# Optimization experiments

Hardware: AMD Instinct MI355X
Metric: run time of the kernel (lower is better)

## Reference

```python
import jax, jax.numpy as jnp
import numpy as np

N = 100000   # total nodes
E = 1000000  # edges
D = 64       # input_dim
H = 128      # embed_dim


def setup_inputs() -> dict:
    key = jax.random.key(0)
    k1, k2, k3, k4 = jax.random.split(key, 4)
    nodes = jnp.arange(N, dtype=jnp.int32)
    features = jax.random.normal(k1, (N, D), dtype=jnp.float32)
    edge_index = jax.random.randint(k2, (2, E), 0, N, dtype=jnp.int32)
    # nn.Linear(2*D, H): weight [H, 2D], bias [H]
    W = jax.random.normal(k3, (H, 2 * D), dtype=jnp.float32) / np.sqrt(2 * D)
    b = jax.random.normal(k4, (H,), dtype=jnp.float32) * 0.01
    return {"nodes": nodes, "features": features, "edge_index": edge_index,
            "W": W, "b": b}


def reference(nodes, features, edge_index, W, b):
    src, dst = edge_index[0], edge_index[1]
    # gcn=False: neighbors are undirected (both src->dst and dst->src).
    # Mean aggregator over all neighbors (full-neighborhood mean).
    ones = jnp.ones((E,), dtype=features.dtype)
    neigh_sum = (jax.ops.segment_sum(features[dst], src, num_segments=N)
                 + jax.ops.segment_sum(features[src], dst, num_segments=N))
    deg = (jax.ops.segment_sum(ones, src, num_segments=N)
           + jax.ops.segment_sum(ones, dst, num_segments=N))
    neigh_mean = neigh_sum / jnp.maximum(deg, 1.0)[:, None]  # [N, D]
    self_feats = features[nodes]            # [B, D]
    neigh_feats = neigh_mean[nodes]         # [B, D]
    combined = jnp.concatenate([self_feats, neigh_feats], axis=1)  # [B, 2D]
    out = jax.nn.relu(combined @ W.T + b)   # [B, H]
    return out
```

## Files before the change

### kernel.cpp

```cpp
#include <hip/hip_runtime.h>
#include <hip/hip_bf16.h>


#define D_IN 64
#define H_OUT 128
#define CAP 64
#define CAP_L 61
#define NPB 32
#define BSHIFT 8
#define BUK_N 256
#define NBUK_MAX 512
#define PASSA_BLOCKS 256
#define PASSA_THREADS 512

typedef unsigned long long ull;
typedef unsigned short ushortt;
typedef unsigned char uchar;
typedef __attribute__((ext_vector_type(8))) short bf16x8;
typedef __attribute__((ext_vector_type(4))) float f32x4;
typedef __attribute__((ext_vector_type(2))) float f32x2;

__device__ __forceinline__ ushortt f2bf(float f) {
    __hip_bfloat16 h = __float2bfloat16(f);
    return *reinterpret_cast<ushortt*>(&h);
}
__device__ __forceinline__ float bf2f(ushortt u) {
    unsigned int x = ((unsigned int)u) << 16;
    return __uint_as_float(x);
}

__global__ __launch_bounds__(PASSA_THREADS) void prep_kernel(
    const int* __restrict__ ei,
    unsigned* __restrict__ gbuf,
    int* __restrict__ blkcnt,
    const float4* __restrict__ feat4,
    const float4* __restrict__ w4,
    ushortt* __restrict__ fb,
    uint2* __restrict__ fq,
    ushortt* __restrict__ Wb,
    int E, int nbuk, int scap, int chunk, int nfeat8, int nw8)
{
    const int t = threadIdx.x;

    if (blockIdx.x >= PASSA_BLOCKS) {
        int i = (blockIdx.x - PASSA_BLOCKS) * PASSA_THREADS + t;
        if (i < nfeat8) {
            float4 a = feat4[2 * i], b = feat4[2 * i + 1];
            bf16x8 o;
            o[0] = (short)f2bf(a.x); o[1] = (short)f2bf(a.y);
            o[2] = (short)f2bf(a.z); o[3] = (short)f2bf(a.w);
            o[4] = (short)f2bf(b.x); o[5] = (short)f2bf(b.y);
            o[6] = (short)f2bf(b.z); o[7] = (short)f2bf(b.w);
            *(bf16x8*)&fb[(size_t)i * 8] = o;
            unsigned lo = (unsigned)__builtin_amdgcn_cvt_pk_fp8_f32(a.x, a.y, 0, false);
            lo = (unsigned)__builtin_amdgcn_cvt_pk_fp8_f32(a.z, a.w, (int)lo, true);
            unsigned hi = (unsigned)__builtin_amdgcn_cvt_pk_fp8_f32(b.x, b.y, 0, false);
            hi = (unsigned)__builtin_amdgcn_cvt_pk_fp8_f32(b.z, b.w, (int)hi, true);
            uint2 q; q.x = lo; q.y = hi;
            fq[i] = q;
        } else {
            int j = i - nfeat8;
            if (j < nw8) {
                float4 a = w4[2 * j], b = w4[2 * j + 1];
                bf16x8 o;
                o[0] = (short)f2bf(a.x); o[1] = (short)f2bf(a.y);
                o[2] = (short)f2bf(a.z); o[3] = (short)f2bf(a.w);
                o[4] = (short)f2bf(b.x); o[5] = (short)f2bf(b.y);
                o[6] = (short)f2bf(b.z); o[7] = (short)f2bf(b.w);
                *(bf16x8*)&Wb[(size_t)j * 8] = o;
            }
        }
        return;
    }

    __shared__ int lcnt[NBUK_MAX];
    for (int i = t; i < nbuk; i += PASSA_THREADS) lcnt[i] = 0;
    __syncthreads();

    const int E2 = 2 * E;
    int lo = blockIdx.x * chunk;
    int hi = lo + chunk; if (hi > E2) hi = E2;

    for (int i = lo + t; i < hi; i += PASSA_THREADS) {
        int u = ei[i];
        int v = (i < E) ? ei[E + i] : ei[i - E];
        int b = u >> BSHIFT;
        unsigned pk = ((unsigned)v << BSHIFT) | (unsigned)(u & (BUK_N - 1));
        int p = atomicAdd(&lcnt[b], 1);
        if (p < scap) gbuf[((size_t)blockIdx.x * nbuk + b) * scap + p] = pk;
    }
    __syncthreads();
    for (int b = t; b < nbuk; b += PASSA_THREADS)
        blkcnt[blockIdx.x * nbuk + b] = lcnt[b];
}

__global__ __launch_bounds__(1024) void adj_agg_kernel(
    const unsigned* __restrict__ gbuf,
    const int* __restrict__ blkcnt,
    const int* __restrict__ ei,
    const uchar* __restrict__ fq,
    ushortt* __restrict__ meanb,
    int N, int E, int nbuk, int scap)
{
    __shared__ unsigned adj_l[BUK_N * CAP_L];
    __shared__ int cnt_l[BUK_N];
    __shared__ int scnt_l[PASSA_BLOCKS];
    __shared__ int satf;

    const int b = blockIdx.x;
    const int t = threadIdx.x;

    if (t == 0) satf = 0;
    if (t < BUK_N) cnt_l[t] = 0;
    if (t < PASSA_BLOCKS) {
        int c = blkcnt[t * nbuk + b];
        scnt_l[t] = c;
        if (c > scap) satf = 1;
    }
    __syncthreads();

    const int wv   = t >> 6;
    const int lane = t & 63;

    if (satf) {
        const int E2 = 2 * E;
        for (int i = t; i < E2; i += 1024) {
            int u = ei[i];
            if ((u >> BSHIFT) != b) continue;
            int v = (i < E) ? ei[E + i] : ei[i - E];
            int ul = u & (BUK_N - 1);
            int p  = atomicAdd(&cnt_l[ul], 1);
            if (p < CAP_L) adj_l[ul * CAP_L + p] = (unsigned)v;
        }
    } else {
        for (int seg = wv; seg < PASSA_BLOCKS; seg += 16) {
            int c = scnt_l[seg]; if (c > scap) c = scap;
            const unsigned* base = gbuf + ((size_t)seg * nbuk + b) * scap;
            for (int i = lane; i < c; i += 64) {
                unsigned e = base[i];
                int ul = e & (BUK_N - 1);
                int v  = (int)(e >> BSHIFT);
                int p  = atomicAdd(&cnt_l[ul], 1);
                if (p < CAP_L) adj_l[ul * CAP_L + p] = (unsigned)v;
            }
        }
    }
    __syncthreads();

    const int oct = lane >> 3;
    const int ol  = lane & 7;
    const uchar* fqb = fq + ol * 8;

    const int nbase = wv * 16;
    const int gbase = (b << BSHIFT) + nbase;

#define GATH(U0, U1, U2, U3, AROW, CC)                                       \
    {                                                                        \
        if ((CC) > 0) {                                                      \
            int jj = oct;      int a = jj < (CC);                            \
            unsigned id = (AROW)[a ? jj : 0];                                \
            U0 = *(const uint2*)(fqb + (size_t)(id * 64u));                  \
            if (!a) { U0.x = 0u; U0.y = 0u; }                                \
        }                                                                    \
        if ((CC) > 8) {                                                      \
            int jj = 8 + oct;  int a = jj < (CC);                            \
            unsigned id = (AROW)[a ? jj : 0];                                \
            U1 = *(const uint2*)(fqb + (size_t)(id * 64u));                  \
            if (!a) { U1.x = 0u; U1.y = 0u; }                                \
        }                                                                    \
        if ((CC) > 16) {                                                     \
            int jj = 16 + oct; int a = jj < (CC);                            \
            unsigned id = (AROW)[a ? jj : 0];                                \
            U2 = *(const uint2*)(fqb + (size_t)(id * 64u));                  \
            if (!a) { U2.x = 0u; U2.y = 0u; }                                \
        }                                                                    \
        if ((CC) > 24) {                                                     \
            int jj = 24 + oct; int a = jj < (CC);                            \
            unsigned id = (AROW)[a ? jj : 0];                                \
            U3 = *(const uint2*)(fqb + (size_t)(id * 64u));                  \
            if (!a) { U3.x = 0u; U3.y = 0u; }                                \
        }                                                                    \
    }

#define DEC(u)                                                       \
    s0 += __builtin_amdgcn_cvt_pk_f32_fp8((int)(u).x, false);        \
    s1 += __builtin_amdgcn_cvt_pk_f32_fp8((int)(u).x, true);         \
    s2 += __builtin_amdgcn_cvt_pk_f32_fp8((int)(u).y, false);        \
    s3 += __builtin_amdgcn_cvt_pk_f32_fp8((int)(u).y, true);

#define FINISH(UA, UB, UC, UD, CC, CTRUE, AROW, G)                           \
    {                                                                        \
        f32x2 s0 = {0.f, 0.f}, s1 = {0.f, 0.f};                              \
        f32x2 s2 = {0.f, 0.f}, s3 = {0.f, 0.f};                              \
        DEC(UA); DEC(UB); DEC(UC); DEC(UD);                                  \
        if (__builtin_expect((CC) > 32, 0)) {                                \
            for (int j = 32; j < (CC); j += 8) {                             \
                int jj = j + oct; int a = jj < (CC);                         \
                unsigned id = (AROW)[a ? jj : 0];                            \
                uint2 u = *(const uint2*)(fqb + (size_t)(id * 64u));         \
                if (!a) { u.x = 0u; u.y = 0u; }                              \
                DEC(u);                                                      \
            }                                                                \
        }                                                                    \
        f32x2 a0, a1;                                                        \
        {                                                                    \
            f32x2 t0, t1, t2, t3;                                            \
            t0.x = __shfl_xor(s0.x, 8);  t0.y = __shfl_xor(s0.y, 8);         \
            t1.x = __shfl_xor(s1.x, 8);  t1.y = __shfl_xor(s1.y, 8);         \
            t2.x = __shfl_xor(s2.x, 8);  t2.y = __shfl_xor(s2.y, 8);         \
            t3.x = __shfl_xor(s3.x, 8);  t3.y = __shfl_xor(s3.y, 8);         \
            bool hi = (oct & 1);                                             \
            a0 = hi ? (s2 + t2) : (s0 + t0);                                 \
            a1 = hi ? (s3 + t3) : (s1 + t1);                                 \
        }                                                                    \
        f32x2 b0;                                                            \
        {                                                                    \
            f32x2 t0, t1;                                                    \
            t0.x = __shfl_xor(a0.x, 16); t0.y = __shfl_xor(a0.y, 16);        \
            t1.x = __shfl_xor(a1.x, 16); t1.y = __shfl_xor(a1.y, 16);        \
            bool hi = (oct & 2);                                             \
            b0 = hi ? (a1 + t1) : (a0 + t0);                                 \
        }                                                                    \
        float cf;                                                            \
        {                                                                    \
            f32x2 tt;                                                        \
            tt.x = __shfl_xor(b0.x, 32); tt.y = __shfl_xor(b0.y, 32);        \
            f32x2 ss = b0 + tt;                                              \
            cf = (oct & 4) ? ss.y : ss.x;                                    \
        }                                                                    \
        float r = 1.0f / fmaxf((float)(CTRUE), 1.0f);                        \
        int d = 8 * ol + 4 * (oct & 1) + (oct & 2) + ((oct >> 2) & 1);       \
        meanb[(size_t)(G) * D_IN + d] = f2bf(cf * r);                        \
    }

    for (int np = 0; np < 8; ++np) {
        const int n0 = nbase + 2 * np;
        const int g0 = gbase + 2 * np;
        const int g1 = g0 + 1;

        const int c0  = (g0 < N) ? cnt_l[n0] : 0;
        const int c1  = (g1 < N) ? cnt_l[n0 + 1] : 0;
        const int cc0 = c0 < CAP_L ? c0 : CAP_L;
        const int cc1 = c1 < CAP_L ? c1 : CAP_L;
        const unsigned* ar0 = &adj_l[n0 * CAP_L];
        const unsigned* ar1 = &adj_l[(n0 + 1) * CAP_L];

        uint2 u00 = {0u,0u}, u01 = {0u,0u}, u02 = {0u,0u}, u03 = {0u,0u};
        uint2 u10 = {0u,0u}, u11 = {0u,0u}, u12 = {0u,0u}, u13 = {0u,0u};
        GATH(u00, u01, u02, u03, ar0, cc0);
        GATH(u10, u11, u12, u13, ar1, cc1);

        if (g0 < N) FINISH(u00, u01, u02, u03, cc0, c0, ar0, g0);
        if (g1 < N) FINISH(u10, u11, u12, u13, cc1, c1, ar1, g1);
    }
#undef GATH
#undef DEC
#undef FINISH
}

__global__ __launch_bounds__(256) void build_adj_kernel(
    const int* __restrict__ ei,
    int* __restrict__ cnt,
    int* __restrict__ adj,
    int E)
{
    const int part   = blockIdx.x & 7;
    const int bloc   = blockIdx.x >> 3;
    const int nbp    = gridDim.x >> 3;
    const int stride = nbp * 256;
    const int E2     = 2 * E;

    for (int i = bloc * 256 + (int)threadIdx.x; i < E2; i += stride) {
        int u = ei[i];
        if (((u >> 4) & 7) != part) continue;
        int v = (i < E) ? ei[E + i] : ei[i - E];
        int p = atomicAdd(&cnt[u], 1);
        if (p < CAP_L) adj[u * CAP + p] = v;
    }
}

__global__ __launch_bounds__(256) void aggregate_f32_kernel(
    const float* __restrict__ feat,
    const int* __restrict__ adj,
    const int* __restrict__ cnt,
    ushortt* __restrict__ meanb,
    int N)
{
    int wid  = (blockIdx.x * blockDim.x + threadIdx.x) >> 6;
    int lane = threadIdx.x & 63;
    if (wid >= N) return;

    int c  = cnt[wid];
    int cc = c < CAP_L ? c : CAP_L;
    int ids = adj[wid * CAP + lane];

    float sum = 0.0f;
    int j = 0;
    for (; j + 8 <= cc; j += 8) {
        int i0 = __shfl(ids, j + 0);
        int i1 = __shfl(ids, j + 1);
        int i2 = __shfl(ids, j + 2);
        int i3 = __shfl(ids, j + 3);
        int i4 = __shfl(ids, j + 4);
        int i5 = __shfl(ids, j + 5);
        int i6 = __shfl(ids, j + 6);
        int i7 = __shfl(ids, j + 7);
        float f0 = feat[i0 * D_IN + lane];
        float f1 = feat[i1 * D_IN + lane];
        float f2 = feat[i2 * D_IN + lane];
        float f3 = feat[i3 * D_IN + lane];
        float f4 = feat[i4 * D_IN + lane];
        float f5 = feat[i5 * D_IN + lane];
        float f6 = feat[i6 * D_IN + lane];
        float f7 = feat[i7 * D_IN + lane];
        sum += ((f0 + f1) + (f2 + f3)) + ((f4 + f5) + (f6 + f7));
    }
    for (; j < cc; ++j)
        sum += feat[__shfl(ids, j) * D_IN + lane];

    float m = sum / fmaxf((float)c, 1.0f);
    meanb[(size_t)wid * D_IN + lane] = f2bf(m);
}

__global__ __launch_bounds__(256) void gemm_mfma_kernel(
    const int* __restrict__ nodes,
    const ushortt* __restrict__ fb,
    const ushortt* __restrict__ meanb,
    const ushortt* __restrict__ Wb,
    const float* __restrict__ bias,
    float* __restrict__ out,
    int N)
{
    __shared__ ushortt w_lds[128 * 136];
    __shared__ int gnode[64];

    const int t  = threadIdx.x;
    const int n0 = blockIdx.x * 64;

    if (t < 64) {
        int idx = n0 + t;
        gnode[t] = nodes[idx < N ? idx : N - 1];
    }
    for (int i = t; i < 128 * 16; i += 256) {
        int row = i >> 4, seg = i & 15;
        *(bf16x8*)&w_lds[row * 136 + seg * 8] =
            *(const bf16x8*)&Wb[row * 128 + seg * 8];
    }
    __syncthreads();

    const int w    = t >> 6;
    const int lane = t & 63;
    const int l15  = lane & 15;
    const int quad = lane >> 4;

    const int g = gnode[w * 16 + l15];
    const bf16x8 a0 = *(const bf16x8*)&fb[(size_t)g * D_IN +  0 + quad * 8];
    const bf16x8 a1 = *(const bf16x8*)&fb[(size_t)g * D_IN + 32 + quad * 8];
    const bf16x8 a2 = *(const bf16x8*)&meanb[(size_t)g * D_IN +  0 + quad * 8];
    const bf16x8 a3 = *(const bf16x8*)&meanb[(size_t)g * D_IN + 32 + quad * 8];

    const int  out_row = n0 + w * 16 + l15;
    const bool valid   = out_row < N;

#pragma unroll
    for (int tile = 0; tile < 8; ++tile) {
        const int h0 = tile * 16;
        const ushortt* wrow = &w_lds[(h0 + l15) * 136];
        bf16x8 b0 = *(const bf16x8*)&wrow[ 0 + quad * 8];
        bf16x8 b1 = *(const bf16x8*)&wrow[32 + quad * 8];
        bf16x8 b2 = *(const bf16x8*)&wrow[64 + quad * 8];
        bf16x8 b3 = *(const bf16x8*)&wrow[96 + quad * 8];

        f32x4 acc = {0.f, 0.f, 0.f, 0.f};
        acc = __builtin_amdgcn_mfma_f32_16x16x32_bf16(b0, a0, acc, 0, 0, 0);
        acc = __builtin_amdgcn_mfma_f32_16x16x32_bf16(b1, a1, acc, 0, 0, 0);
        acc = __builtin_amdgcn_mfma_f32_16x16x32_bf16(b2, a2, acc, 0, 0, 0);
        acc = __builtin_amdgcn_mfma_f32_16x16x32_bf16(b3, a3, acc, 0, 0, 0);

        if (valid) {
            float4 bv = *(const float4*)&bias[h0 + quad * 4];
            float4 o;
            o.x = fmaxf(acc[0] + bv.x, 0.0f);
            o.y = fmaxf(acc[1] + bv.y, 0.0f);
            o.z = fmaxf(acc[2] + bv.z, 0.0f);
            o.w = fmaxf(acc[3] + bv.w, 0.0f);
            *(float4*)&out[(size_t)out_row * H_OUT + h0 + quad * 4] = o;
        }
    }
}

__global__ __launch_bounds__(256) void gemm_kernel(
    const int* __restrict__ nodes,
    const float* __restrict__ feat,
    const ushortt* __restrict__ meanb,
    const float* __restrict__ W,
    const float* __restrict__ bias,
    float* __restrict__ out,
    int N)
{
    __shared__ float w_lds[64 * 132];
    __shared__ float comb_self[NPB * 68];
    __shared__ float comb_mean[NPB * 68];
    __shared__ int   gnode[NPB];

    const int t  = threadIdx.x;
    const int n0 = blockIdx.x * NPB;

    if (t < NPB) {
        int idx = n0 + t;
        if (idx >= N) idx = N - 1;
        gnode[t] = nodes[idx];
    }
    __syncthreads();

    for (int i = t; i < NPB * 64; i += 256) {
        int n = i >> 6, d = i & 63;
        int g = gnode[n];
        comb_self[n * 68 + d] = feat[g * D_IN + d];
        comb_mean[n * 68 + d] = bf2f(meanb[(size_t)g * D_IN + d]);
    }
    for (int i = t; i < H_OUT * 64; i += 256) {
        int h = i >> 6, kk = i & 63;
        w_lds[kk * 132 + h] = W[h * (2 * D_IN) + kk];
    }
    __syncthreads();

    const int tx = t & 31;
    const int ty = t >> 5;
    const int h0 = tx * 4;
    const int nl = ty * 4;

    float acc[4][4];
#pragma unroll
    for (int j = 0; j < 4; j++)
#pragma unroll
        for (int i = 0; i < 4; i++) acc[j][i] = 0.0f;

    for (int kk = 0; kk < 64; kk += 4) {
        float4 wvv[4], cv[4];
#pragma unroll
        for (int i = 0; i < 4; i++)
            wvv[i] = *(const float4*)&w_lds[(kk + i) * 132 + h0];
#pragma unroll
        for (int j = 0; j < 4; j++)
            cv[j] = *(const float4*)&comb_self[(nl + j) * 68 + kk];
#pragma unroll
        for (int j = 0; j < 4; j++) {
            const float* c = (const float*)&cv[j];
#pragma unroll
            for (int i = 0; i < 4; i++) {
                const float* wp = (const float*)&wvv[i];
                acc[j][0] += wp[0] * c[i];
                acc[j][1] += wp[1] * c[i];
                acc[j][2] += wp[2] * c[i];
                acc[j][3] += wp[3] * c[i];
            }
        }
    }
    __syncthreads();

    for (int i = t; i < H_OUT * 64; i += 256) {
        int h = i >> 6, kk = i & 63;
        w_lds[kk * 132 + h] = W[h * (2 * D_IN) + 64 + kk];
    }
    __syncthreads();

    for (int kk = 0; kk < 64; kk += 4) {
        float4 wvv[4], cv[4];
#pragma unroll
        for (int i = 0; i < 4; i++)
            wvv[i] = *(const float4*)&w_lds[(kk + i) * 132 + h0];
#pragma unroll
        for (int j = 0; j < 4; j++)
            cv[j] = *(const float4*)&comb_mean[(nl + j) * 68 + kk];
#pragma unroll
        for (int j = 0; j < 4; j++) {
            const float* c = (const float*)&cv[j];
#pragma unroll
            for (int i = 0; i < 4; i++) {
                const float* wp = (const float*)&wvv[i];
                acc[j][0] += wp[0] * c[i];
                acc[j][1] += wp[1] * c[i];
                acc[j][2] += wp[2] * c[i];
                acc[j][3] += wp[3] * c[i];
            }
        }
    }

    float4 bv = *(const float4*)&bias[h0];
#pragma unroll
    for (int j = 0; j < 4; j++) {
        int n = n0 + nl + j;
        if (n >= N) continue;
        float4 o;
        o.x = fmaxf(acc[j][0] + bv.x, 0.0f);
        o.y = fmaxf(acc[j][1] + bv.y, 0.0f);
        o.z = fmaxf(acc[j][2] + bv.z, 0.0f);
        o.w = fmaxf(acc[j][3] + bv.w, 0.0f);
        *(float4*)&out[(size_t)n * H_OUT + h0] = o;
    }
}

extern "C" void kernel_launch(void* const* d_in, const int* in_sizes, int n_in,
                              void* d_out, int out_size, void* d_ws, size_t ws_size,
                              hipStream_t stream) {
    const int*   nodes = (const int*)d_in[0];
    const float* feat  = (const float*)d_in[1];
    const int*   ei    = (const int*)d_in[2];
    const float* W     = (const float*)d_in[3];
    const float* bias  = (const float*)d_in[4];
    float*       out   = (float*)d_out;

    const int N  = in_sizes[0];
    const int E  = in_sizes[2] / 2;
    const int E2 = 2 * E;

    const int nbuk  = (N + BUK_N - 1) >> BSHIFT;
    const int chunk = (E2 + PASSA_BLOCKS - 1) / PASSA_BLOCKS;
    double ex = (double)chunk * (double)BUK_N / (double)N;
    int scap = ((int)(ex + 9.0 * __builtin_sqrt(ex)) + 31) & ~15;
    if (scap < 64) scap = 64;

    char* base = (char*)d_ws;
    size_t off = 0;
    auto aln = [](size_t x) { return (x + 63) & ~(size_t)63; };
    int*     cnt    = (int*)(base + off);     off = aln(off + (size_t)N * 4);
    int*     adj    = (int*)(base + off);     off = aln(off + (size_t)N * CAP * 4);
    ushortt* meanb  = (ushortt*)(base + off); off = aln(off + (size_t)N * D_IN * 2);
    int*     blkcnt = (int*)(base + off);     off = aln(off + (size_t)PASSA_BLOCKS * NBUK_MAX * 4);
    ushortt* Wb     = (ushortt*)(base + off); off = aln(off + (size_t)H_OUT * 2 * D_IN * 2);
    ushortt* fb     = (ushortt*)(base + off); off = aln(off + (size_t)N * D_IN * 2);
    uchar*   fq     = (uchar*)(base + off);   off = aln(off + (size_t)N * D_IN);
    unsigned* gbuf  = (unsigned*)(base + off);
    const size_t total = off + (size_t)PASSA_BLOCKS * nbuk * scap * 4;

    const bool full = (N <= 131072) && (nbuk <= NBUK_MAX) && (ws_size >= total)
                   && ((N * D_IN) % 8 == 0);

    if (full) {
        const int nfeat8 = N * D_IN / 8;
        const int nw8    = H_OUT * 2 * D_IN / 8;
        const int conv_blocks = (nfeat8 + nw8 + PASSA_THREADS - 1) / PASSA_THREADS;
        prep_kernel<<<PASSA_BLOCKS + conv_blocks, PASSA_THREADS, 0, stream>>>(
            ei, gbuf, blkcnt, (const float4*)feat, (const float4*)W,
            fb, (uint2*)fq, Wb, E, nbuk, scap, chunk, nfeat8, nw8);
        adj_agg_kernel<<<nbuk, 1024, 0, stream>>>(gbuf, blkcnt, ei, fq,
                                                  meanb, N, E, nbuk, scap);
        gemm_mfma_kernel<<<(N + 63) / 64, 256, 0, stream>>>(
            nodes, fb, meanb, Wb, bias, out, N);
    } else {
        const int ablocks = (int)(((size_t)N * 64 + 255) / 256);
        hipMemsetAsync(cnt, 0, (size_t)N * sizeof(int), stream);
        build_adj_kernel<<<2048, 256, 0, stream>>>(ei, cnt, adj, E);
        aggregate_f32_kernel<<<ablocks, 256, 0, stream>>>(feat, adj, cnt,
                                                          meanb, N);
        gemm_kernel<<<(N + NPB - 1) / NPB, 256, 0, stream>>>(
            nodes, feat, meanb, W, bias, out, N);
    }
}
```

Measured before the change: 169.9 us.

## Fuse output GEMM into aggregation kernel with identity-nodes fast path and backup

```diff
diff --git a/kernel.cpp b/kernel.cpp
--- a/kernel.cpp
+++ b/kernel.cpp
@@ -38,9 +38,11 @@
     ushortt* __restrict__ fb,
     uint2* __restrict__ fq,
     ushortt* __restrict__ Wb,
+    int* __restrict__ flag,
     int E, int nbuk, int scap, int chunk, int nfeat8, int nw8)
 {
     const int t = threadIdx.x;
+    if (blockIdx.x == 0 && t == 0) *flag = 0;
 
     if (blockIdx.x >= PASSA_BLOCKS) {
         int i = (blockIdx.x - PASSA_BLOCKS) * PASSA_THREADS + t;
@@ -94,12 +96,18 @@
         blkcnt[blockIdx.x * nbuk + b] = lcnt[b];
 }
 
-__global__ __launch_bounds__(1024) void adj_agg_kernel(
+__global__ __launch_bounds__(1024, 8) void adj_agg_kernel(
     const unsigned* __restrict__ gbuf,
     const int* __restrict__ blkcnt,
     const int* __restrict__ ei,
     const uchar* __restrict__ fq,
     ushortt* __restrict__ meanb,
+    const int* __restrict__ nodes,
+    const ushortt* __restrict__ fb,
+    const ushortt* __restrict__ Wb,
+    const float* __restrict__ bias,
+    float* __restrict__ out,
+    int* __restrict__ flag,
     int N, int E, int nbuk, int scap)
 {
     __shared__ unsigned adj_l[BUK_N * CAP_L];
@@ -256,6 +264,128 @@
 #undef GATH
 #undef DEC
 #undef FINISH
+
+    __threadfence();
+    __syncthreads();
+    {
+        const int grp   = t >> 8;
+        const int t256  = t & 255;
+        const int w2    = t256 >> 6;
+        const int lane2 = t256 & 63;
+        const int l15   = lane2 & 15;
+        const int quad  = lane2 >> 4;
+
+        const int out_row = (b << BSHIFT) + grp * 64 + w2 * 16 + l15;
+        const bool valid  = out_row < N;
+        const int g       = valid ? out_row : N - 1;
+
+        int nv = nodes[g];
+        bool okl = (!valid) || (nv == out_row);
+        if (!__all(okl)) {
+            if (lane2 == 0) atomicOr(flag, 1);
+        } else {
+            const bf16x8 a0 = *(const bf16x8*)&fb[(size_t)g * D_IN +  0 + quad * 8];
+            const bf16x8 a1 = *(const bf16x8*)&fb[(size_t)g * D_IN + 32 + quad * 8];
+            const bf16x8 a2 = *(const bf16x8*)&meanb[(size_t)g * D_IN +  0 + quad * 8];
+            const bf16x8 a3 = *(const bf16x8*)&meanb[(size_t)g * D_IN + 32 + quad * 8];
+
+#pragma unroll
+            for (int tile = 0; tile < 8; ++tile) {
+                const int h0 = tile * 16;
+                const ushortt* wrow = &Wb[(size_t)(h0 + l15) * 128];
+                bf16x8 b0 = *(const bf16x8*)&wrow[ 0 + quad * 8];
+                bf16x8 b1 = *(const bf16x8*)&wrow[32 + quad * 8];
+                bf16x8 b2 = *(const bf16x8*)&wrow[64 + quad * 8];
+                bf16x8 b3 = *(const bf16x8*)&wrow[96 + quad * 8];
+
+                f32x4 acc = {0.f, 0.f, 0.f, 0.f};
+                acc = __builtin_amdgcn_mfma_f32_16x16x32_bf16(b0, a0, acc, 0, 0, 0);
+                acc = __builtin_amdgcn_mfma_f32_16x16x32_bf16(b1, a1, acc, 0, 0, 0);
+                acc = __builtin_amdgcn_mfma_f32_16x16x32_bf16(b2, a2, acc, 0, 0, 0);
+                acc = __builtin_amdgcn_mfma_f32_16x16x32_bf16(b3, a3, acc, 0, 0, 0);
+
+                if (valid) {
+                    float4 bv = *(const float4*)&bias[h0 + quad * 4];
+                    float4 o;
+                    o.x = fmaxf(acc[0] + bv.x, 0.0f);
+                    o.y = fmaxf(acc[1] + bv.y, 0.0f);
+                    o.z = fmaxf(acc[2] + bv.z, 0.0f);
+                    o.w = fmaxf(acc[3] + bv.w, 0.0f);
+                    *(float4*)&out[(size_t)out_row * H_OUT + h0 + quad * 4] = o;
+                }
+            }
+        }
+    }
+}
+
+__global__ __launch_bounds__(256) void gemm_backup_kernel(
+    const int* __restrict__ nodes,
+    const ushortt* __restrict__ fb,
+    const ushortt* __restrict__ meanb,
+    const ushortt* __restrict__ Wb,
+    const float* __restrict__ bias,
+    float* __restrict__ out,
+    const int* __restrict__ flag,
+    int N)
+{
+    if (*flag == 0) return;
+
+    __shared__ ushortt w_lds[128 * 136];
+    __shared__ int gnode[64];
+
+    const int t  = threadIdx.x;
+    const int n0 = blockIdx.x * 64;
+
+    if (t < 64) {
+        int idx = n0 + t;
+        gnode[t] = nodes[idx < N ? idx : N - 1];
+    }
+    for (int i = t; i < 128 * 16; i += 256) {
+        int row = i >> 4, seg = i & 15;
+        *(bf16x8*)&w_lds[row * 136 + seg * 8] =
+            *(const bf16x8*)&Wb[row * 128 + seg * 8];
+    }
+    __syncthreads();
+
+    const int w    = t >> 6;
+    const int lane = t & 63;
+    const int l15  = lane & 15;
+    const int quad = lane >> 4;
+
+    const int g = gnode[w * 16 + l15];
+    const bf16x8 a0 = *(const bf16x8*)&fb[(size_t)g * D_IN +  0 + quad * 8];
+    const bf16x8 a1 = *(const bf16x8*)&fb[(size_t)g * D_IN + 32 + quad * 8];
+    const bf16x8 a2 = *(const bf16x8*)&meanb[(size_t)g * D_IN +  0 + quad * 8];
+    const bf16x8 a3 = *(const bf16x8*)&meanb[(size_t)g * D_IN + 32 + quad * 8];
+
+    const int  out_row = n0 + w * 16 + l15;
+    const bool valid   = out_row < N;
+
+#pragma unroll
+    for (int tile = 0; tile < 8; ++tile) {
+        const int h0 = tile * 16;
+        const ushortt* wrow = &w_lds[(h0 + l15) * 136];
+        bf16x8 b0 = *(const bf16x8*)&wrow[ 0 + quad * 8];
+        bf16x8 b1 = *(const bf16x8*)&wrow[32 + quad * 8];
+        bf16x8 b2 = *(const bf16x8*)&wrow[64 + quad * 8];
+        bf16x8 b3 = *(const bf16x8*)&wrow[96 + quad * 8];
+
+        f32x4 acc = {0.f, 0.f, 0.f, 0.f};
+        acc = __builtin_amdgcn_mfma_f32_16x16x32_bf16(b0, a0, acc, 0, 0, 0);
+        acc = __builtin_amdgcn_mfma_f32_16x16x32_bf16(b1, a1, acc, 0, 0, 0);
+        acc = __builtin_amdgcn_mfma_f32_16x16x32_bf16(b2, a2, acc, 0, 0, 0);
+        acc = __builtin_amdgcn_mfma_f32_16x16x32_bf16(b3, a3, acc, 0, 0, 0);
+
+        if (valid) {
+            float4 bv = *(const float4*)&bias[h0 + quad * 4];
+            float4 o;
+            o.x = fmaxf(acc[0] + bv.x, 0.0f);
+            o.y = fmaxf(acc[1] + bv.y, 0.0f);
+            o.z = fmaxf(acc[2] + bv.z, 0.0f);
+            o.w = fmaxf(acc[3] + bv.w, 0.0f);
+            *(float4*)&out[(size_t)out_row * H_OUT + h0 + quad * 4] = o;
+        }
+    }
 }
 
 __global__ __launch_bounds__(256) void build_adj_kernel(
@@ -322,73 +452,6 @@
     meanb[(size_t)wid * D_IN + lane] = f2bf(m);
 }
 
-__global__ __launch_bounds__(256) void gemm_mfma_kernel(
-    const int* __restrict__ nodes,
-    const ushortt* __restrict__ fb,
-    const ushortt* __restrict__ meanb,
-    const ushortt* __restrict__ Wb,
-    const float* __restrict__ bias,
-    float* __restrict__ out,
-    int N)
-{
-    __shared__ ushortt w_lds[128 * 136];
-    __shared__ int gnode[64];
-
-    const int t  = threadIdx.x;
-    const int n0 = blockIdx.x * 64;
-
-    if (t < 64) {
-        int idx = n0 + t;
-        gnode[t] = nodes[idx < N ? idx : N - 1];
-    }
-    for (int i = t; i < 128 * 16; i += 256) {
-        int row = i >> 4, seg = i & 15;
-        *(bf16x8*)&w_lds[row * 136 + seg * 8] =
-            *(const bf16x8*)&Wb[row * 128 + seg * 8];
-    }
-    __syncthreads();
-
-    const int w    = t >> 6;
-    const int lane = t & 63;
-    const int l15  = lane & 15;
-    const int quad = lane >> 4;
-
-    const int g = gnode[w * 16 + l15];
-    const bf16x8 a0 = *(const bf16x8*)&fb[(size_t)g * D_IN +  0 + quad * 8];
-    const bf16x8 a1 = *(const bf16x8*)&fb[(size_t)g * D_IN + 32 + quad * 8];
-    const bf16x8 a2 = *(const bf16x8*)&meanb[(size_t)g * D_IN +  0 + quad * 8];
-    const bf16x8 a3 = *(const bf16x8*)&meanb[(size_t)g * D_IN + 32 + quad * 8];
-
-    const int  out_row = n0 + w * 16 + l15;
-    const bool valid   = out_row < N;
-
-#pragma unroll
-    for (int tile = 0; tile < 8; ++tile) {
-        const int h0 = tile * 16;
-        const ushortt* wrow = &w_lds[(h0 + l15) * 136];
-        bf16x8 b0 = *(const bf16x8*)&wrow[ 0 + quad * 8];
-        bf16x8 b1 = *(const bf16x8*)&wrow[32 + quad * 8];
-        bf16x8 b2 = *(const bf16x8*)&wrow[64 + quad * 8];
-        bf16x8 b3 = *(const bf16x8*)&wrow[96 + quad * 8];
-
-        f32x4 acc = {0.f, 0.f, 0.f, 0.f};
-        acc = __builtin_amdgcn_mfma_f32_16x16x32_bf16(b0, a0, acc, 0, 0, 0);
-        acc = __builtin_amdgcn_mfma_f32_16x16x32_bf16(b1, a1, acc, 0, 0, 0);
-        acc = __builtin_amdgcn_mfma_f32_16x16x32_bf16(b2, a2, acc, 0, 0, 0);
-        acc = __builtin_amdgcn_mfma_f32_16x16x32_bf16(b3, a3, acc, 0, 0, 0);
-
-        if (valid) {
-            float4 bv = *(const float4*)&bias[h0 + quad * 4];
-            float4 o;
-            o.x = fmaxf(acc[0] + bv.x, 0.0f);
-            o.y = fmaxf(acc[1] + bv.y, 0.0f);
-            o.z = fmaxf(acc[2] + bv.z, 0.0f);
-            o.w = fmaxf(acc[3] + bv.w, 0.0f);
-            *(float4*)&out[(size_t)out_row * H_OUT + h0 + quad * 4] = o;
-        }
-    }
-}
-
 __global__ __launch_bounds__(256) void gemm_kernel(
     const int* __restrict__ nodes,
     const float* __restrict__ feat,
@@ -528,6 +591,7 @@
     int*     adj    = (int*)(base + off);     off = aln(off + (size_t)N * CAP * 4);
     ushortt* meanb  = (ushortt*)(base + off); off = aln(off + (size_t)N * D_IN * 2);
     int*     blkcnt = (int*)(base + off);     off = aln(off + (size_t)PASSA_BLOCKS * NBUK_MAX * 4);
+    int*     flag   = (int*)(base + off);     off = aln(off + 64);
     ushortt* Wb     = (ushortt*)(base + off); off = aln(off + (size_t)H_OUT * 2 * D_IN * 2);
     ushortt* fb     = (ushortt*)(base + off); off = aln(off + (size_t)N * D_IN * 2);
     uchar*   fq     = (uchar*)(base + off);   off = aln(off + (size_t)N * D_IN);
@@ -543,11 +607,12 @@
         const int conv_blocks = (nfeat8 + nw8 + PASSA_THREADS - 1) / PASSA_THREADS;
         prep_kernel<<<PASSA_BLOCKS + conv_blocks, PASSA_THREADS, 0, stream>>>(
             ei, gbuf, blkcnt, (const float4*)feat, (const float4*)W,
-            fb, (uint2*)fq, Wb, E, nbuk, scap, chunk, nfeat8, nw8);
-        adj_agg_kernel<<<nbuk, 1024, 0, stream>>>(gbuf, blkcnt, ei, fq,
-                                                  meanb, N, E, nbuk, scap);
-        gemm_mfma_kernel<<<(N + 63) / 64, 256, 0, stream>>>(
-            nodes, fb, meanb, Wb, bias, out, N);
+            fb, (uint2*)fq, Wb, flag, E, nbuk, scap, chunk, nfeat8, nw8);
+        adj_agg_kernel<<<nbuk, 1024, 0, stream>>>(
+            gbuf, blkcnt, ei, fq, meanb, nodes, fb, Wb, bias, out, flag,
+            N, E, nbuk, scap);
+        gemm_backup_kernel<<<(N + 63) / 64, 256, 0, stream>>>(
+            nodes, fb, meanb, Wb, bias, out, flag, N);
     } else {
         const int ablocks = (int)(((size_t)N * 64 + 255) / 256);
         hipMemsetAsync(cnt, 0, (size_t)N * sizeof(int), stream);
```

Measured after the change: 371.3 us. +118.6%, slower.
